# Kernel tuning notes

Measured on AMD Instinct MI355X. Metric: run time of the kernel, lower is better.

## Reference

```python
import jax, jax.numpy as jnp
import numpy as np

S_SIGMA = 8      # spatial downsampling of the bilateral grid
N_BINS = 16      # intensity bins (range resolution)
EPS = 1e-8


def _blur_axis(g, k, axis):
    """1D correlation of grid g with small tap filter k along `axis` (zero pad)."""
    taps = k.shape[0]
    r = taps // 2
    pad = [(0, 0)] * g.ndim
    pad[axis] = (r, r)
    gp = jnp.pad(g, pad)
    n = g.shape[axis]
    out = k[0] * jax.lax.slice_in_dim(gp, 0, n, axis=axis)
    for i in range(1, taps):
        out = out + k[i] * jax.lax.slice_in_dim(gp, i, i + n, axis=axis)
    return out


def _bilateral_one(img, fs, fr):
    """Bilateral grid splat -> blur -> slice for a single [H,W] channel.
    Guide signal is the channel itself (values assumed in [0,1])."""
    H, W = img.shape
    GH = (H - 1) // S_SIGMA + 2
    GW = (W - 1) // S_SIGMA + 2
    GZ = N_BINS + 1

    ys = jnp.arange(H, dtype=img.dtype)
    xs = jnp.arange(W, dtype=img.dtype)

    # ---- splat (nearest-cell scatter-add of homogeneous (value, weight)) ----
    gy = jnp.round(ys / S_SIGMA).astype(jnp.int32)            # [H]
    gx = jnp.round(xs / S_SIGMA).astype(jnp.int32)            # [W]
    gyg, gxg = jnp.meshgrid(gy, gx, indexing='ij')            # [H,W]
    gz = jnp.clip(jnp.round(img * (N_BINS - 1)), 0, N_BINS - 1).astype(jnp.int32)
    val = jnp.zeros((GH, GW, GZ), img.dtype).at[gyg, gxg, gz].add(img)
    wt = jnp.zeros((GH, GW, GZ), img.dtype).at[gyg, gxg, gz].add(jnp.ones_like(img))

    # ---- blur grid: learnable 5-tap filter_s along y,x and filter_r along z ----
    for axis, k in ((0, fs), (1, fs), (2, fr)):
        val = _blur_axis(val, k, axis)
        wt = _blur_axis(wt, k, axis)

    # ---- slice (trilinear gather at (y/s, x/s, I*(NB-1))) ----
    fy = ys / S_SIGMA
    fx = xs / S_SIGMA
    fz = jnp.clip(img * (N_BINS - 1), 0.0, N_BINS - 1)        # [H,W]
    y0 = jnp.floor(fy).astype(jnp.int32)
    x0 = jnp.floor(fx).astype(jnp.int32)
    z0 = jnp.floor(fz).astype(jnp.int32)
    y1 = jnp.minimum(y0 + 1, GH - 1)
    x1 = jnp.minimum(x0 + 1, GW - 1)
    z1 = jnp.minimum(z0 + 1, GZ - 1)
    ty = fy - y0.astype(img.dtype)                            # [H]
    tx = fx - x0.astype(img.dtype)                            # [W]
    tz = fz - z0.astype(img.dtype)                            # [H,W]

    out_v = jnp.zeros_like(img)
    out_w = jnp.zeros_like(img)
    for yi, wy in ((y0, 1.0 - ty), (y1, ty)):
        for xi, wx in ((x0, 1.0 - tx), (x1, tx)):
            for zi, wz in ((z0, 1.0 - tz), (z1, tz)):
                w = wy[:, None] * wx[None, :] * wz            # [H,W]
                out_v = out_v + w * val[yi[:, None], xi[None, :], zi]
                out_w = out_w + w * wt[yi[:, None], xi[None, :], zi]
    return out_v / (out_w + EPS)


def setup_inputs() -> dict:
    key = jax.random.key(0)
    k1, k2 = jax.random.split(key)
    blurred_batch = jax.random.uniform(k1, (4, 3, 1024, 1024), dtype=jnp.float32)
    kernel_batch = jax.random.uniform(k2, (4, 11, 11), dtype=jnp.float32)
    g = jnp.array([1.0, 4.0, 6.0, 4.0, 1.0], dtype=jnp.float32)
    g = g / g.sum()  # smooth 5-tap filter so the blur is nontrivial
    return {
        'blurred_batch': blurred_batch,
        'kernel_batch': kernel_batch,
        'filter_s': g,
        'filter_r': g,
        'num_irls_iter': 1,
        'num_cg_iter': 5,
    }


def reference(blurred_batch, kernel_batch, filter_s, filter_r, num_irls_iter, num_cg_iter):
    # kernel_batch, num_irls_iter, num_cg_iter are unused on this code path,
    # matching the original forward (only BilateralGrid.apply touches x).
    B, C, H, W = blurred_batch.shape
    imgs = blurred_batch.reshape(B * C, H, W)
    out = jax.vmap(lambda im: _bilateral_one(im, filter_s, filter_r))(imgs)
    return out.reshape(B, C, H, W)
```

## Files before the change

kernel.cpp:

```cpp
#include <hip/hip_runtime.h>

#define S_SIGMA 8
#define NBINS   16
#define HDIM    1024
#define WDIM    1024
#define GH      129
#define GW      129
#define GZ      17
#define CELLS   (GH*GW*GZ)
#define ROWSZ   (GW*GZ)
#define EPSV    1e-8f
#define FIXS    1048576.0f
#define FIXI    (1.0f/1048576.0f)

__global__ __launch_bounds__(256) void splat_gather_kernel(
    const float* __restrict__ img, float* __restrict__ grid, int nImg, int imgBase)
{
    __shared__ unsigned lval[16 * 64];
    __shared__ unsigned lwt [16 * 64];

    int tid = threadIdx.x;
    int c   = tid & 63;
    int q   = tid >> 6;
    int cellIdx = blockIdx.x * 64 + c;
    int total = nImg * GH * GW;

    for (int i = tid; i < 16 * 64; i += 256) { lval[i] = 0u; lwt[i] = 0u; }
    __syncthreads();

    if (cellIdx < total) {
        int b   = cellIdx / (GH * GW);
        int rem = cellIdx - b * (GH * GW);
        int gy  = rem / GW;
        int gx  = rem - gy * GW;
        const float* ib = img + (size_t)(imgBase + b) * (HDIM * WDIM);

        bool interior = (gx >= 1) & (gx <= 127) & (gy >= 1) & (gy <= 127);
        if (interior) {
            int py = gy & 1, px = gx & 1;
            int ylo = 8 * gy - 4 + py;
            int nr  = 9 - 2 * py;
            int ax  = 8 * gx - 4;
            for (int r = q; r < nr; r += 4) {
                const float* rp = ib + (size_t)(ylo + r) * WDIM + ax;
                float4 A = *(const float4*)rp;
                float4 B = *(const float4*)(rp + 4);
                float  cv = rp[8];
                float e7[7] = {A.y, A.z, A.w, B.x, B.y, B.z, B.w};
                #pragma unroll
                for (int j = 0; j < 7; ++j) {
                    float v = e7[j];
                    int gz = min(max((int)rintf(v * 15.0f), 0), 15);
                    atomicAdd(&lval[gz * 64 + c], (unsigned)rintf(v * FIXS));
                    atomicAdd(&lwt [gz * 64 + c], 1u);
                }
                if (!px) {
                    int gz = min(max((int)rintf(A.x * 15.0f), 0), 15);
                    atomicAdd(&lval[gz * 64 + c], (unsigned)rintf(A.x * FIXS));
                    atomicAdd(&lwt [gz * 64 + c], 1u);
                    gz = min(max((int)rintf(cv * 15.0f), 0), 15);
                    atomicAdd(&lval[gz * 64 + c], (unsigned)rintf(cv * FIXS));
                    atomicAdd(&lwt [gz * 64 + c], 1u);
                }
            }
        } else {
            int ylo = max(0, 8 * gy - 4 + (gy & 1));
            int yhi = min(HDIM - 1, 8 * gy + 4 - (gy & 1));
            int xlo = max(0, 8 * gx - 4 + (gx & 1));
            int xhi = min(WDIM - 1, 8 * gx + 4 - (gx & 1));
            for (int y = ylo + q; y <= yhi; y += 4) {
                const float* row = ib + (size_t)y * WDIM;
                for (int x = xlo; x <= xhi; ++x) {
                    float v = row[x];
                    int gz = min(max((int)rintf(v * 15.0f), 0), 15);
                    atomicAdd(&lval[gz * 64 + c], (unsigned)rintf(v * FIXS));
                    atomicAdd(&lwt [gz * 64 + c], 1u);
                }
            }
        }
    }
    __syncthreads();

    if (cellIdx < total) {
        float2* dst = (float2*)grid + (size_t)cellIdx * GZ;
        int zlo = q * 4;
        int zhi = (q == 3) ? 17 : zlo + 4;
        for (int z = zlo; z < zhi; ++z) {
            float2 o;
            if (z == 16) { o.x = 0.f; o.y = 0.f; }
            else {
                o.x = (float)lval[z * 64 + c] * FIXI;
                o.y = (float)lwt [z * 64 + c];
            }
            dst[z] = o;
        }
    }
}

#define TO 12
#define TI 16
#define NIN  (TI*TI*GZ)
#define NTMP (TO*TI*GZ)
#define NOUT (TO*TO*GZ)
#define NTI  13
#define NXI  10

__global__ __launch_bounds__(256) void blur_fused_kernel(
    const float2* __restrict__ in, float2* __restrict__ out,
    const float* __restrict__ kfs, const float* __restrict__ kfr)
{
    __shared__ float2 sbin[NIN];

    int tid = threadIdx.x;
    int tx0 = blockIdx.x * TO;
    int ty0 = blockIdx.y * TO;
    int b   = blockIdx.z;

    float ks[5] = {kfs[0], kfs[1], kfs[2], kfs[3], kfs[4]};
    float kr[5] = {kfr[0], kfr[1], kfr[2], kfr[3], kfr[4]};

    const float2* gb = in + (size_t)b * CELLS;
    for (int li = tid; li < NIN; li += 256) {
        int iy = li / (TI * GZ);
        int r  = li - iy * (TI * GZ);
        int ix = r / GZ;
        int z  = r - ix * GZ;
        int gy = ty0 - 2 + iy;
        int gx = tx0 - 2 + ix;
        float2 v; v.x = 0.f; v.y = 0.f;
        if (gy >= 0 && gy < GH && gx >= 0 && gx < GW)
            v = gb[((size_t)gy * GW + gx) * GZ + z];
        sbin[li] = v;
    }
    __syncthreads();

    float2 rt[NTI];
    #pragma unroll
    for (int it = 0; it < NTI; ++it) {
        int o = tid + it * 256;
        float2 a; a.x = 0.f; a.y = 0.f;
        if (o < NTMP) {
            int oy = o / (TI * GZ);
            int r  = o - oy * (TI * GZ);
            #pragma unroll
            for (int t = 0; t < 5; ++t) {
                float2 g = sbin[(oy + t) * (TI * GZ) + r];
                a.x += ks[t] * g.x;
                a.y += ks[t] * g.y;
            }
        }
        rt[it] = a;
    }
    __syncthreads();
    #pragma unroll
    for (int it = 0; it < NTI; ++it) {
        int o = tid + it * 256;
        if (o < NTMP) sbin[o] = rt[it];
    }
    __syncthreads();

    float2 rx[NXI];
    #pragma unroll
    for (int it = 0; it < NXI; ++it) {
        int o = tid + it * 256;
        float2 a; a.x = 0.f; a.y = 0.f;
        if (o < NOUT) {
            int oy = o / (TO * GZ);
            int r  = o - oy * (TO * GZ);
            int ox = r / GZ;
            int z  = r - ox * GZ;
            #pragma unroll
            for (int t = 0; t < 5; ++t) {
                float2 g = sbin[(oy * TI + ox + t) * GZ + z];
                a.x += ks[t] * g.x;
                a.y += ks[t] * g.y;
            }
        }
        rx[it] = a;
    }
    __syncthreads();
    #pragma unroll
    for (int it = 0; it < NXI; ++it) {
        int o = tid + it * 256;
        if (o < NOUT) sbin[o] = rx[it];
    }
    __syncthreads();

    float2* ob = out + (size_t)b * CELLS;
    for (int o = tid; o < NOUT; o += 256) {
        int oy = o / (GZ * TO);
        int r2 = o - oy * (GZ * TO);
        int z  = r2 / TO;
        int ox = r2 - z * TO;
        int gy = ty0 + oy;
        int gx = tx0 + ox;
        if (gy < GH && gx < GW) {
            int cb = (oy * TO + ox) * GZ;
            float2 a; a.x = 0.f; a.y = 0.f;
            #pragma unroll
            for (int t = 0; t < 5; ++t) {
                int zz = z + t - 2;
                if (zz >= 0 && zz < GZ) {
                    float2 g = sbin[cb + zz];
                    a.x += kr[t] * g.x;
                    a.y += kr[t] * g.y;
                }
            }
            ob[((size_t)gy * GZ + z) * GW + gx] = a;
        }
    }
}

#define XP2   136
#define RST   XP2
#define ZST   (2*XP2)

__global__ __launch_bounds__(256) void slice_rows_kernel(
    const float* __restrict__ img, const float2* __restrict__ grid,
    float* __restrict__ out, int imgBase)
{
    __shared__ float2 sg[GZ * ZST];

    int tid = threadIdx.x;
    int k   = blockIdx.x;
    int b   = blockIdx.y;

    const float2* gsrc = grid + (size_t)b * CELLS + (size_t)k * ROWSZ;
    for (int i = tid; i < 2 * ROWSZ; i += 256) {
        int r   = i / ROWSZ;
        int rem = i - r * ROWSZ;
        int z   = rem / GW;
        int x0  = rem - z * GW;
        sg[z * ZST + r * RST + x0] = gsrc[i];
    }
    __syncthreads();

    int x   = tid << 2;
    int x0v = tid >> 1;
    float txb = (float)(x & 7) * 0.125f;

    size_t rowBase = (size_t)(imgBase + b) * (HDIM * WDIM) + (size_t)(k << 3) * WDIM + x;

    #pragma unroll
    for (int r = 0; r < 8; ++r) {
        size_t pixBase = rowBase + (size_t)r * WDIM;
        float4 v4 = *(const float4*)(img + pixBase);
        float ty = (float)r * 0.125f;
        float wy0 = 1.f - ty, wy1 = ty;

        float vv[4] = {v4.x, v4.y, v4.z, v4.w};
        float rr[4];
        #pragma unroll
        for (int j = 0; j < 4; ++j) {
            float v  = vv[j];
            float fz = fminf(fmaxf(v * 15.0f, 0.0f), 15.0f);
            float zf = floorf(fz);
            int   z0 = (int)zf;
            float tz = fz - zf;
            float tx = txb + (float)j * 0.125f;
            float wx0 = 1.f - tx, wx1 = tx;
            float wz0 = 1.f - tz, wz1 = tz;

            int base = z0 * ZST + x0v;
            float2 g000 = sg[base];
            float2 g010 = sg[base + 1];
            float2 g100 = sg[base + RST];
            float2 g110 = sg[base + RST + 1];
            float2 g001 = sg[base + ZST];
            float2 g011 = sg[base + ZST + 1];
            float2 g101 = sg[base + ZST + RST];
            float2 g111 = sg[base + ZST + RST + 1];

            float ov = 0.f, ow = 0.f, w;
            w = wy0 * wx0 * wz0; ov += w * g000.x; ow += w * g000.y;
            w = wy0 * wx0 * wz1; ov += w * g001.x; ow += w * g001.y;
            w = wy0 * wx1 * wz0; ov += w * g010.x; ow += w * g010.y;
            w = wy0 * wx1 * wz1; ov += w * g011.x; ow += w * g011.y;
            w = wy1 * wx0 * wz0; ov += w * g100.x; ow += w * g100.y;
            w = wy1 * wx0 * wz1; ov += w * g101.x; ow += w * g101.y;
            w = wy1 * wx1 * wz0; ov += w * g110.x; ow += w * g110.y;
            w = wy1 * wx1 * wz1; ov += w * g111.x; ow += w * g111.y;
            rr[j] = ov / (ow + EPSV);
        }
        float4 r4; r4.x = rr[0]; r4.y = rr[1]; r4.z = rr[2]; r4.w = rr[3];
        *(float4*)(out + pixBase) = r4;
    }
}

extern "C" void kernel_launch(void* const* d_in, const int* in_sizes, int n_in,
                              void* d_out, int out_size, void* d_ws, size_t ws_size,
                              hipStream_t stream)
{
    const float* img = (const float*)d_in[0];
    const float* fs  = (const float*)d_in[2];
    const float* fr  = (const float*)d_in[3];
    float* out = (float*)d_out;

    int nImgTotal = in_sizes[0] / (HDIM * WDIM);
    size_t perImgBytes = (size_t)CELLS * 2 * sizeof(float);

    int maxChunk = (int)(ws_size / (2 * perImgBytes));
    if (maxChunk < 1) return;
    if (maxChunk > nImgTotal) maxChunk = nImgTotal;

    const int tilesPerDim = (GH + TO - 1) / TO;

    for (int base = 0; base < nImgTotal; base += maxChunk) {
        int c = nImgTotal - base;
        if (c > maxChunk) c = maxChunk;

        float* A = (float*)d_ws;
        float* B = A + (size_t)c * CELLS * 2;

        int nCells = c * GH * GW;
        int cellBlocks = (nCells + 63) / 64;
        splat_gather_kernel<<<cellBlocks, 256, 0, stream>>>(img, A, c, base);

        dim3 bgrid(tilesPerDim, tilesPerDim, c);
        blur_fused_kernel<<<bgrid, 256, 0, stream>>>((const float2*)A, (float2*)B, fs, fr);

        dim3 sgrid(HDIM / 8, c);
        slice_rows_kernel<<<sgrid, 256, 0, stream>>>(img, (const float2*)B, out, base);
    }
}
```

Before: 93.43 us.

## Replace per-cell gather splat with pixel-tile scatter splat using global atomics

```diff
diff --git a/kernel.cpp b/kernel.cpp
--- a/kernel.cpp
+++ b/kernel.cpp
@@ -12,87 +12,55 @@
 #define EPSV    1e-8f
 #define FIXS    1048576.0f
 #define FIXI    (1.0f/1048576.0f)
-
-__global__ __launch_bounds__(256) void splat_gather_kernel(
-    const float* __restrict__ img, float* __restrict__ grid, int nImg, int imgBase)
-{
-    __shared__ unsigned lval[16 * 64];
-    __shared__ unsigned lwt [16 * 64];
+#define LCELLS  (9*9*16)
+
+__global__ __launch_bounds__(256) void splat_tile_kernel(
+    const float* __restrict__ img, float* __restrict__ grid, int imgBase)
+{
+    __shared__ unsigned lval[LCELLS];
+    __shared__ unsigned lwt [LCELLS];
 
     int tid = threadIdx.x;
-    int c   = tid & 63;
-    int q   = tid >> 6;
-    int cellIdx = blockIdx.x * 64 + c;
-    int total = nImg * GH * GW;
-
-    for (int i = tid; i < 16 * 64; i += 256) { lval[i] = 0u; lwt[i] = 0u; }
-    __syncthreads();
-
-    if (cellIdx < total) {
-        int b   = cellIdx / (GH * GW);
-        int rem = cellIdx - b * (GH * GW);
-        int gy  = rem / GW;
-        int gx  = rem - gy * GW;
-        const float* ib = img + (size_t)(imgBase + b) * (HDIM * WDIM);
-
-        bool interior = (gx >= 1) & (gx <= 127) & (gy >= 1) & (gy <= 127);
-        if (interior) {
-            int py = gy & 1, px = gx & 1;
-            int ylo = 8 * gy - 4 + py;
-            int nr  = 9 - 2 * py;
-            int ax  = 8 * gx - 4;
-            for (int r = q; r < nr; r += 4) {
-                const float* rp = ib + (size_t)(ylo + r) * WDIM + ax;
-                float4 A = *(const float4*)rp;
-                float4 B = *(const float4*)(rp + 4);
-                float  cv = rp[8];
-                float e7[7] = {A.y, A.z, A.w, B.x, B.y, B.z, B.w};
-                #pragma unroll
-                for (int j = 0; j < 7; ++j) {
-                    float v = e7[j];
-                    int gz = min(max((int)rintf(v * 15.0f), 0), 15);
-                    atomicAdd(&lval[gz * 64 + c], (unsigned)rintf(v * FIXS));
-                    atomicAdd(&lwt [gz * 64 + c], 1u);
-                }
-                if (!px) {
-                    int gz = min(max((int)rintf(A.x * 15.0f), 0), 15);
-                    atomicAdd(&lval[gz * 64 + c], (unsigned)rintf(A.x * FIXS));
-                    atomicAdd(&lwt [gz * 64 + c], 1u);
-                    gz = min(max((int)rintf(cv * 15.0f), 0), 15);
-                    atomicAdd(&lval[gz * 64 + c], (unsigned)rintf(cv * FIXS));
-                    atomicAdd(&lwt [gz * 64 + c], 1u);
-                }
-            }
-        } else {
-            int ylo = max(0, 8 * gy - 4 + (gy & 1));
-            int yhi = min(HDIM - 1, 8 * gy + 4 - (gy & 1));
-            int xlo = max(0, 8 * gx - 4 + (gx & 1));
-            int xhi = min(WDIM - 1, 8 * gx + 4 - (gx & 1));
-            for (int y = ylo + q; y <= yhi; y += 4) {
-                const float* row = ib + (size_t)y * WDIM;
-                for (int x = xlo; x <= xhi; ++x) {
-                    float v = row[x];
-                    int gz = min(max((int)rintf(v * 15.0f), 0), 15);
-                    atomicAdd(&lval[gz * 64 + c], (unsigned)rintf(v * FIXS));
-                    atomicAdd(&lwt [gz * 64 + c], 1u);
-                }
-            }
-        }
-    }
-    __syncthreads();
-
-    if (cellIdx < total) {
-        float2* dst = (float2*)grid + (size_t)cellIdx * GZ;
-        int zlo = q * 4;
-        int zhi = (q == 3) ? 17 : zlo + 4;
-        for (int z = zlo; z < zhi; ++z) {
-            float2 o;
-            if (z == 16) { o.x = 0.f; o.y = 0.f; }
-            else {
-                o.x = (float)lval[z * 64 + c] * FIXI;
-                o.y = (float)lwt [z * 64 + c];
-            }
-            dst[z] = o;
+    int tx  = blockIdx.x;
+    int ty  = blockIdx.y;
+    int b   = blockIdx.z;
+
+    for (int i = tid; i < LCELLS; i += 256) { lval[i] = 0u; lwt[i] = 0u; }
+    __syncthreads();
+
+    const float* ib = img + (size_t)(imgBase + b) * (HDIM * WDIM)
+                        + (size_t)(ty * 64) * WDIM + tx * 64;
+
+    #pragma unroll
+    for (int it = 0; it < 4; ++it) {
+        int p   = it * 256 + tid;
+        int ly  = p >> 4;
+        int lx4 = p & 15;
+        float4 v4 = *(const float4*)(ib + (size_t)ly * WDIM + lx4 * 4);
+        int gyl = (int)rintf((float)ly * 0.125f);
+        float vv[4] = {v4.x, v4.y, v4.z, v4.w};
+        #pragma unroll
+        for (int j = 0; j < 4; ++j) {
+            float v = vv[j];
+            int gxl = (int)rintf((float)(lx4 * 4 + j) * 0.125f);
+            int gz  = min(max((int)rintf(v * 15.0f), 0), 15);
+            int bin = (gyl * 9 + gxl) * 16 + gz;
+            atomicAdd(&lval[bin], (unsigned)rintf(v * FIXS));
+            atomicAdd(&lwt [bin], 1u);
+        }
+    }
+    __syncthreads();
+
+    for (int i = tid; i < LCELLS; i += 256) {
+        unsigned w = lwt[i];
+        if (w) {
+            int gyl = i / 144;
+            int rem = i - gyl * 144;
+            int gxl = rem >> 4;
+            int gz  = rem & 15;
+            size_t cell = (((size_t)b * GH + ty * 8 + gyl) * GW + tx * 8 + gxl) * GZ + gz;
+            atomicAdd(&grid[2 * cell],     (float)lval[i] * FIXI);
+            atomicAdd(&grid[2 * cell + 1], (float)w);
         }
     }
 }
@@ -312,9 +280,10 @@
         float* A = (float*)d_ws;
         float* B = A + (size_t)c * CELLS * 2;
 
-        int nCells = c * GH * GW;
-        int cellBlocks = (nCells + 63) / 64;
-        splat_gather_kernel<<<cellBlocks, 256, 0, stream>>>(img, A, c, base);
+        hipMemsetAsync(A, 0, (size_t)c * perImgBytes, stream);
+
+        dim3 sgrid2(16, 16, c);
+        splat_tile_kernel<<<sgrid2, 256, 0, stream>>>(img, A, base);
 
         dim3 bgrid(tilesPerDim, tilesPerDim, c);
         blur_fused_kernel<<<bgrid, 256, 0, stream>>>((const float2*)A, (float2*)B, fs, fr);
```

Result: slower. 136.9 us (+46.5%).

## Split blur tiles along z into two halves with smaller spatial tiles

Applied to the files above, without the earlier changes.

```diff
diff --git a/kernel.cpp b/kernel.cpp
--- a/kernel.cpp
+++ b/kernel.cpp
@@ -97,54 +97,60 @@
     }
 }
 
-#define TO 12
-#define TI 16
-#define NIN  (TI*TI*GZ)
-#define NTMP (TO*TI*GZ)
-#define NOUT (TO*TO*GZ)
-#define NTI  13
-#define NXI  10
-
-__global__ __launch_bounds__(256) void blur_fused_kernel(
+#define TO 8
+#define TI 12
+#define NZI_MAX 11
+#define NTI 5
+#define NXI 3
+
+__global__ __launch_bounds__(256, 8) void blur_fused_kernel(
     const float2* __restrict__ in, float2* __restrict__ out,
     const float* __restrict__ kfs, const float* __restrict__ kfr)
 {
-    __shared__ float2 sbin[NIN];
+    __shared__ float2 sbin[TI * TI * NZI_MAX];
 
     int tid = threadIdx.x;
     int tx0 = blockIdx.x * TO;
-    int ty0 = blockIdx.y * TO;
+    int h   = blockIdx.y & 1;
+    int ty0 = (blockIdx.y >> 1) * TO;
     int b   = blockIdx.z;
+
+    int zbase = h * 7;
+    int nzi   = 11 - h;
+    int nzo   = 9 - h;
+    int zolo  = 9 * h;
 
     float ks[5] = {kfs[0], kfs[1], kfs[2], kfs[3], kfs[4]};
     float kr[5] = {kfr[0], kfr[1], kfr[2], kfr[3], kfr[4]};
 
     const float2* gb = in + (size_t)b * CELLS;
-    for (int li = tid; li < NIN; li += 256) {
-        int iy = li / (TI * GZ);
-        int r  = li - iy * (TI * GZ);
-        int ix = r / GZ;
-        int z  = r - ix * GZ;
+    int nin = TI * TI * nzi;
+    for (int li = tid; li < nin; li += 256) {
+        int iy = li / (TI * nzi);
+        int r  = li - iy * (TI * nzi);
+        int ix = r / nzi;
+        int zi = r - ix * nzi;
         int gy = ty0 - 2 + iy;
         int gx = tx0 - 2 + ix;
         float2 v; v.x = 0.f; v.y = 0.f;
         if (gy >= 0 && gy < GH && gx >= 0 && gx < GW)
-            v = gb[((size_t)gy * GW + gx) * GZ + z];
+            v = gb[((size_t)gy * GW + gx) * GZ + zbase + zi];
         sbin[li] = v;
     }
     __syncthreads();
 
+    int ntmp = TO * TI * nzi;
     float2 rt[NTI];
     #pragma unroll
     for (int it = 0; it < NTI; ++it) {
         int o = tid + it * 256;
         float2 a; a.x = 0.f; a.y = 0.f;
-        if (o < NTMP) {
-            int oy = o / (TI * GZ);
-            int r  = o - oy * (TI * GZ);
+        if (o < ntmp) {
+            int oy = o / (TI * nzi);
+            int r  = o - oy * (TI * nzi);
             #pragma unroll
             for (int t = 0; t < 5; ++t) {
-                float2 g = sbin[(oy + t) * (TI * GZ) + r];
+                float2 g = sbin[(oy + t) * (TI * nzi) + r];
                 a.x += ks[t] * g.x;
                 a.y += ks[t] * g.y;
             }
@@ -155,23 +161,24 @@
     #pragma unroll
     for (int it = 0; it < NTI; ++it) {
         int o = tid + it * 256;
-        if (o < NTMP) sbin[o] = rt[it];
-    }
-    __syncthreads();
-
+        if (o < ntmp) sbin[o] = rt[it];
+    }
+    __syncthreads();
+
+    int nx = TO * TO * nzi;
     float2 rx[NXI];
     #pragma unroll
     for (int it = 0; it < NXI; ++it) {
         int o = tid + it * 256;
         float2 a; a.x = 0.f; a.y = 0.f;
-        if (o < NOUT) {
-            int oy = o / (TO * GZ);
-            int r  = o - oy * (TO * GZ);
-            int ox = r / GZ;
-            int z  = r - ox * GZ;
+        if (o < nx) {
+            int oy = o / (TO * nzi);
+            int r  = o - oy * (TO * nzi);
+            int ox = r / nzi;
+            int zi = r - ox * nzi;
             #pragma unroll
             for (int t = 0; t < 5; ++t) {
-                float2 g = sbin[(oy * TI + ox + t) * GZ + z];
+                float2 g = sbin[oy * (TI * nzi) + (ox + t) * nzi + zi];
                 a.x += ks[t] * g.x;
                 a.y += ks[t] * g.y;
             }
@@ -182,31 +189,33 @@
     #pragma unroll
     for (int it = 0; it < NXI; ++it) {
         int o = tid + it * 256;
-        if (o < NOUT) sbin[o] = rx[it];
+        if (o < nx) sbin[o] = rx[it];
     }
     __syncthreads();
 
     float2* ob = out + (size_t)b * CELLS;
-    for (int o = tid; o < NOUT; o += 256) {
-        int oy = o / (GZ * TO);
-        int r2 = o - oy * (GZ * TO);
-        int z  = r2 / TO;
-        int ox = r2 - z * TO;
+    int nout = TO * TO * nzo;
+    for (int o = tid; o < nout; o += 256) {
+        int oy = o / (nzo * TO);
+        int r2 = o - oy * (nzo * TO);
+        int k  = r2 / TO;
+        int ox = r2 - k * TO;
+        int zo = zolo + k;
         int gy = ty0 + oy;
         int gx = tx0 + ox;
         if (gy < GH && gx < GW) {
-            int cb = (oy * TO + ox) * GZ;
+            int cb = (oy * TO + ox) * nzi;
             float2 a; a.x = 0.f; a.y = 0.f;
             #pragma unroll
             for (int t = 0; t < 5; ++t) {
-                int zz = z + t - 2;
-                if (zz >= 0 && zz < GZ) {
-                    float2 g = sbin[cb + zz];
+                int zg = zo + t - 2;
+                if (zg >= 0 && zg <= 16) {
+                    float2 g = sbin[cb + zg - zbase];
                     a.x += kr[t] * g.x;
                     a.y += kr[t] * g.y;
                 }
             }
-            ob[((size_t)gy * GZ + z) * GW + gx] = a;
+            ob[((size_t)gy * GZ + zo) * GW + gx] = a;
         }
     }
 }
@@ -316,7 +325,7 @@
         int cellBlocks = (nCells + 63) / 64;
         splat_gather_kernel<<<cellBlocks, 256, 0, stream>>>(img, A, c, base);
 
-        dim3 bgrid(tilesPerDim, tilesPerDim, c);
+        dim3 bgrid(tilesPerDim, tilesPerDim * 2, c);
         blur_fused_kernel<<<bgrid, 256, 0, stream>>>((const float2*)A, (float2*)B, fs, fr);
 
         dim3 sgrid(HDIM / 8, c);
```

Measured after the change: 95.24 us. About the same (+1.9%).

## Split fused blur into separate y-pass and register-based xz-pass kernels

Applied to the files above, without the earlier changes.

```diff
diff --git a/kernel.cpp b/kernel.cpp
--- a/kernel.cpp
+++ b/kernel.cpp
@@ -97,117 +97,77 @@
     }
 }
 
-#define TO 12
-#define TI 16
-#define NIN  (TI*TI*GZ)
-#define NTMP (TO*TI*GZ)
-#define NOUT (TO*TO*GZ)
-#define NTI  13
-#define NXI  10
-
-__global__ __launch_bounds__(256) void blur_fused_kernel(
+__global__ __launch_bounds__(256) void blur_y_row(
+    const float2* __restrict__ in, float2* __restrict__ out,
+    const float* __restrict__ kfs)
+{
+    int i  = blockIdx.x * 256 + threadIdx.x;
+    if (i >= ROWSZ) return;
+    int gy = blockIdx.y;
+    int b  = blockIdx.z;
+
+    float ks[5] = {kfs[0], kfs[1], kfs[2], kfs[3], kfs[4]};
+
+    const float2* gb = in + (size_t)b * CELLS + i;
+    float2 a; a.x = 0.f; a.y = 0.f;
+    #pragma unroll
+    for (int t = 0; t < 5; ++t) {
+        int yy = gy + t - 2;
+        if (yy >= 0 && yy < GH) {
+            float2 g = gb[(size_t)yy * ROWSZ];
+            a.x += ks[t] * g.x;
+            a.y += ks[t] * g.y;
+        }
+    }
+    out[(size_t)b * CELLS + (size_t)gy * ROWSZ + i] = a;
+}
+
+__global__ __launch_bounds__(256) void blur_xz_col(
     const float2* __restrict__ in, float2* __restrict__ out,
     const float* __restrict__ kfs, const float* __restrict__ kfr)
 {
-    __shared__ float2 sbin[NIN];
-
-    int tid = threadIdx.x;
-    int tx0 = blockIdx.x * TO;
-    int ty0 = blockIdx.y * TO;
-    int b   = blockIdx.z;
+    int rem = blockIdx.x * 256 + threadIdx.x;
+    if (rem >= GH * GW) return;
+    int b  = blockIdx.y;
+    int gy = rem / GW;
+    int gx = rem - gy * GW;
 
     float ks[5] = {kfs[0], kfs[1], kfs[2], kfs[3], kfs[4]};
     float kr[5] = {kfr[0], kfr[1], kfr[2], kfr[3], kfr[4]};
 
-    const float2* gb = in + (size_t)b * CELLS;
-    for (int li = tid; li < NIN; li += 256) {
-        int iy = li / (TI * GZ);
-        int r  = li - iy * (TI * GZ);
-        int ix = r / GZ;
-        int z  = r - ix * GZ;
-        int gy = ty0 - 2 + iy;
-        int gx = tx0 - 2 + ix;
-        float2 v; v.x = 0.f; v.y = 0.f;
-        if (gy >= 0 && gy < GH && gx >= 0 && gx < GW)
-            v = gb[((size_t)gy * GW + gx) * GZ + z];
-        sbin[li] = v;
-    }
-    __syncthreads();
-
-    float2 rt[NTI];
-    #pragma unroll
-    for (int it = 0; it < NTI; ++it) {
-        int o = tid + it * 256;
+    float2 xb[GZ];
+    #pragma unroll
+    for (int z = 0; z < GZ; ++z) { xb[z].x = 0.f; xb[z].y = 0.f; }
+
+    const float2* gb = in + (size_t)b * CELLS + (size_t)gy * ROWSZ;
+    #pragma unroll
+    for (int t = 0; t < 5; ++t) {
+        int xx = gx + t - 2;
+        if (xx >= 0 && xx < GW) {
+            const float2* col = gb + (size_t)xx * GZ;
+            float k = ks[t];
+            #pragma unroll
+            for (int z = 0; z < GZ; ++z) {
+                float2 g = col[z];
+                xb[z].x += k * g.x;
+                xb[z].y += k * g.y;
+            }
+        }
+    }
+
+    float2* ob = out + (size_t)b * CELLS + (size_t)gy * ROWSZ + gx;
+    #pragma unroll
+    for (int z = 0; z < GZ; ++z) {
         float2 a; a.x = 0.f; a.y = 0.f;
-        if (o < NTMP) {
-            int oy = o / (TI * GZ);
-            int r  = o - oy * (TI * GZ);
-            #pragma unroll
-            for (int t = 0; t < 5; ++t) {
-                float2 g = sbin[(oy + t) * (TI * GZ) + r];
-                a.x += ks[t] * g.x;
-                a.y += ks[t] * g.y;
-            }
-        }
-        rt[it] = a;
-    }
-    __syncthreads();
-    #pragma unroll
-    for (int it = 0; it < NTI; ++it) {
-        int o = tid + it * 256;
-        if (o < NTMP) sbin[o] = rt[it];
-    }
-    __syncthreads();
-
-    float2 rx[NXI];
-    #pragma unroll
-    for (int it = 0; it < NXI; ++it) {
-        int o = tid + it * 256;
-        float2 a; a.x = 0.f; a.y = 0.f;
-        if (o < NOUT) {
-            int oy = o / (TO * GZ);
-            int r  = o - oy * (TO * GZ);
-            int ox = r / GZ;
-            int z  = r - ox * GZ;
-            #pragma unroll
-            for (int t = 0; t < 5; ++t) {
-                float2 g = sbin[(oy * TI + ox + t) * GZ + z];
-                a.x += ks[t] * g.x;
-                a.y += ks[t] * g.y;
-            }
-        }
-        rx[it] = a;
-    }
-    __syncthreads();
-    #pragma unroll
-    for (int it = 0; it < NXI; ++it) {
-        int o = tid + it * 256;
-        if (o < NOUT) sbin[o] = rx[it];
-    }
-    __syncthreads();
-
-    float2* ob = out + (size_t)b * CELLS;
-    for (int o = tid; o < NOUT; o += 256) {
-        int oy = o / (GZ * TO);
-        int r2 = o - oy * (GZ * TO);
-        int z  = r2 / TO;
-        int ox = r2 - z * TO;
-        int gy = ty0 + oy;
-        int gx = tx0 + ox;
-        if (gy < GH && gx < GW) {
-            int cb = (oy * TO + ox) * GZ;
-            float2 a; a.x = 0.f; a.y = 0.f;
-            #pragma unroll
-            for (int t = 0; t < 5; ++t) {
-                int zz = z + t - 2;
-                if (zz >= 0 && zz < GZ) {
-                    float2 g = sbin[cb + zz];
-                    a.x += kr[t] * g.x;
-                    a.y += kr[t] * g.y;
-                }
-            }
-            ob[((size_t)gy * GZ + z) * GW + gx] = a;
-        }
+        #pragma unroll
+        for (int t = 0; t < 5; ++t) {
+            int zz = z + t - 2;
+            if (zz >= 0 && zz < GZ) {
+                a.x += kr[t] * xb[zz].x;
+                a.y += kr[t] * xb[zz].y;
+            }
+        }
+        ob[(size_t)z * GW] = a;
     }
 }
 
@@ -303,8 +263,6 @@
     if (maxChunk < 1) return;
     if (maxChunk > nImgTotal) maxChunk = nImgTotal;
 
-    const int tilesPerDim = (GH + TO - 1) / TO;
-
     for (int base = 0; base < nImgTotal; base += maxChunk) {
         int c = nImgTotal - base;
         if (c > maxChunk) c = maxChunk;
@@ -316,10 +274,13 @@
         int cellBlocks = (nCells + 63) / 64;
         splat_gather_kernel<<<cellBlocks, 256, 0, stream>>>(img, A, c, base);
 
-        dim3 bgrid(tilesPerDim, tilesPerDim, c);
-        blur_fused_kernel<<<bgrid, 256, 0, stream>>>((const float2*)A, (float2*)B, fs, fr);
+        dim3 ygrid((ROWSZ + 255) / 256, GH, c);
+        blur_y_row<<<ygrid, 256, 0, stream>>>((const float2*)A, (float2*)B, fs);
+
+        dim3 xzgrid((GH * GW + 255) / 256, c);
+        blur_xz_col<<<xzgrid, 256, 0, stream>>>((const float2*)B, (float2*)A, fs, fr);
 
         dim3 sgrid(HDIM / 8, c);
-        slice_rows_kernel<<<sgrid, 256, 0, stream>>>(img, (const float2*)B, out, base);
-    }
-}
+        slice_rows_kernel<<<sgrid, 256, 0, stream>>>(img, (const float2*)A, out, base);
+    }
+}
```

Result: slower. 109.7 us, median of 2 (+17.4%).
